# Kernel tuning notes

Hardware: AMD Instinct MI355X
Metric: run time of the kernel (lower is better)

## Reference

```python
import jax, jax.numpy as jnp
import numpy as np
import math

NUM_HEADS = 16
ATTN_WIDTH = 256


def setup_inputs() -> dict:
    key = jax.random.key(0)
    ks = jax.random.split(key, 5)
    B, S, C, H = 2, 2048, 1024, 1024
    scale = 0.02
    return {
        "x": jax.random.normal(ks[0], (B, S, C), dtype=jnp.float32),
        "Wq": jax.random.normal(ks[1], (C, H), dtype=jnp.float32) * scale,
        "Wk": jax.random.normal(ks[2], (C, H), dtype=jnp.float32) * scale,
        "Wv": jax.random.normal(ks[3], (C, H), dtype=jnp.float32) * scale,
        "Wo": jax.random.normal(ks[4], (H, C), dtype=jnp.float32) * scale,
    }


def reference(x, Wq, Wk, Wv, Wo):
    B, S, C = x.shape
    H = NUM_HEADS
    dh = Wq.shape[1] // H  # head dim; Q.size(-1) in torch code

    def split_heads(t):
        # [B, S, H*dh] -> [B, H, S, dh]
        return t.reshape(B, S, H, dh).transpose(0, 2, 1, 3)

    q = split_heads(x @ Wq)
    k = split_heads(x @ Wk)
    v = split_heads(x @ Wv)

    scores = jnp.einsum("bhqd,bhkd->bhqk", q, k) / math.sqrt(dh)
    # exp-shift (first 'softmax-like' step, unnormalized)
    scores = jnp.exp(scores - jnp.max(scores, axis=-1, keepdims=True))
    # banded mask: tril(attn_width//2 - 1).triu(-(attn_width//2))
    i = jnp.arange(S)[:, None]
    j = jnp.arange(S)[None, :]
    d = j - i
    half = ATTN_WIDTH // 2
    mask = (d <= half - 1) & (d >= -half)
    scores = jnp.where(mask, scores, 0.0)
    # second softmax over the masked exp-scores (zeros contribute exp(0)=1)
    weights = jax.nn.softmax(scores, axis=-1)

    out = jnp.einsum("bhqk,bhkd->bhqd", weights, v)  # [B, H, S, dh]
    out = out.transpose(0, 2, 1, 3).reshape(B, S, H * dh)
    return out @ Wo
```

## Files before the change

kernel.cpp:

```cpp
#include <hip/hip_runtime.h>
#include <math.h>

typedef __bf16 bf16_t;
typedef bf16_t bf16x8 __attribute__((ext_vector_type(8)));
typedef bf16_t bf16x4 __attribute__((ext_vector_type(4)));
typedef float f32x4 __attribute__((ext_vector_type(4)));

constexpr int S_ = 2048;
constexpr float SCALE = 0.125f;

#define MFMA_B16(a, b, c) __builtin_amdgcn_mfma_f32_16x16x32_bf16(a, b, c, 0, 0, 0)

#define WAIT_VM0() __builtin_amdgcn_s_waitcnt(0x0F70)
#define WAIT_VM2() __builtin_amdgcn_s_waitcnt(0x0F72)
#define WAIT_VM4() __builtin_amdgcn_s_waitcnt(0x0F74)
#define BARRIER()  __builtin_amdgcn_s_barrier()

typedef __attribute__((address_space(1))) const void* as1_cvp;
typedef __attribute__((address_space(3))) void* as3_vp;

__device__ __forceinline__ void gl2lds16(const void* g, void* l)
{
    __builtin_amdgcn_global_load_lds((as1_cvp)g, (as3_vp)l, 16, 0, 0);
}

#define SRC_SWZ8(lane) ((((lane) & 3) ^ (((lane) >> 3) & 3)) * 8)
#define RD_SWZ8(quad, l15) ((((quad) ^ (((l15) >> 1) & 3))) * 8)

__global__ __launch_bounds__(256) void prep(const float* __restrict__ x,
                                            const float* __restrict__ Wq,
                                            const float* __restrict__ Wk,
                                            const float* __restrict__ Wv,
                                            const float* __restrict__ Wo,
                                            bf16_t* __restrict__ xb,
                                            bf16_t* __restrict__ Wqt,
                                            bf16_t* __restrict__ Wkt,
                                            bf16_t* __restrict__ Wvt,
                                            bf16_t* __restrict__ Wot,
                                            float* __restrict__ vsp)
{
    __shared__ float T[64][65];
    const int blk = blockIdx.x;
    const int tid = threadIdx.x;
    if (blk < 1024) {
#pragma unroll
        for (int u = 0; u < 4; ++u) {
            const int g = blk * 1024 + u * 256 + tid;
            const float4 v = ((const float4*)x)[g];
            bf16x4 o;
            o[0] = (bf16_t)v.x; o[1] = (bf16_t)v.y;
            o[2] = (bf16_t)v.z; o[3] = (bf16_t)v.w;
            *(bf16x4*)&xb[(size_t)g * 4] = o;
        }
    } else if (blk < 2048) {
        const int rem = blk - 1024;
        const int wsel = rem >> 8, t = rem & 255;
        const float* src = (wsel == 0) ? Wq : (wsel == 1) ? Wk : (wsel == 2) ? Wv : Wo;
        bf16_t* dst = (wsel == 0) ? Wqt : (wsel == 1) ? Wkt : (wsel == 2) ? Wvt : Wot;
        const int k0 = (t >> 4) * 64, n0 = (t & 15) * 64;
        const int rr = tid >> 4, c4 = (tid & 15) * 4;
#pragma unroll
        for (int u = 0; u < 4; ++u) {
            const float4 v = *(const float4*)&src[(size_t)(k0 + u * 16 + rr) * 1024 + n0 + c4];
            T[u * 16 + rr][c4 + 0] = v.x; T[u * 16 + rr][c4 + 1] = v.y;
            T[u * 16 + rr][c4 + 2] = v.z; T[u * 16 + rr][c4 + 3] = v.w;
        }
        __syncthreads();
#pragma unroll
        for (int u = 0; u < 4; ++u) {
            bf16x4 o;
#pragma unroll
            for (int e = 0; e < 4; ++e) o[e] = (bf16_t)T[c4 + e][u * 16 + rr];
            *(bf16x4*)&dst[(size_t)(n0 + u * 16 + rr) * 1024 + k0 + c4] = o;
        }
    } else {
#pragma unroll
        for (int u = 0; u < 8; ++u) vsp[u * 256 + tid] = 0.f;
    }
}

template <int MODE>
__device__ __forceinline__ void mfma_gemm_body(bf16_t* __restrict__ As,
                                               bf16_t* __restrict__ Bs,
                                               const bf16_t* __restrict__ A,
                                               const bf16_t* __restrict__ Bt,
                                               void* __restrict__ dst,
                                               float* __restrict__ vsum_out,
                                               int m0, int n0)
{
    const int tid = threadIdx.x;
    const int lane = tid & 63, wid = tid >> 6;
    const int l15 = lane & 15, quad = lane >> 4;
    const int wm = (wid & 1) * 64, wn = (wid >> 1) * 64;

    const int srow = wid * 32 + (lane >> 2);
    const int scg8 = SRC_SWZ8(lane);
    const bf16_t* Ag0 = A  + (size_t)(m0 + srow) * 1024 + scg8;
    const bf16_t* Ag1 = A  + (size_t)(m0 + srow + 16) * 1024 + scg8;
    const bf16_t* Bg0 = Bt + (size_t)(n0 + srow) * 1024 + scg8;
    const bf16_t* Bg1 = Bt + (size_t)(n0 + srow + 16) * 1024 + scg8;

    const int rs = RD_SWZ8(quad, l15);

    f32x4 acc[4][4];
#pragma unroll
    for (int i = 0; i < 4; ++i)
#pragma unroll
        for (int j = 0; j < 4; ++j) acc[i][j] = (f32x4){0.f, 0.f, 0.f, 0.f};

#pragma unroll
    for (int p = 0; p < 2; ++p) {
        const int k0 = p * 32;
        gl2lds16(Ag0 + k0, As + p * 4096 + (wid * 2 + 0) * 512);
        gl2lds16(Ag1 + k0, As + p * 4096 + (wid * 2 + 1) * 512);
        gl2lds16(Bg0 + k0, Bs + p * 4096 + (wid * 2 + 0) * 512);
        gl2lds16(Bg1 + k0, Bs + p * 4096 + (wid * 2 + 1) * 512);
    }

#pragma unroll
    for (int it = 0; it < 32; ++it) {
        if (it < 30) WAIT_VM4(); else WAIT_VM0();
        BARRIER();
        if (it < 30) {
            const int k0 = (it + 2) * 32;
            const int sb = (it + 2) % 3;
            gl2lds16(Ag0 + k0, As + sb * 4096 + (wid * 2 + 0) * 512);
            gl2lds16(Ag1 + k0, As + sb * 4096 + (wid * 2 + 1) * 512);
            gl2lds16(Bg0 + k0, Bs + sb * 4096 + (wid * 2 + 0) * 512);
            gl2lds16(Bg1 + k0, Bs + sb * 4096 + (wid * 2 + 1) * 512);
        }
        const int cb = it % 3;
        bf16x8 af[4], bfr[4];
#pragma unroll
        for (int mt = 0; mt < 4; ++mt)
            af[mt] = *(const bf16x8*)&As[cb * 4096 + (wm + mt * 16 + l15) * 32 + rs];
#pragma unroll
        for (int nt = 0; nt < 4; ++nt)
            bfr[nt] = *(const bf16x8*)&Bs[cb * 4096 + (wn + nt * 16 + l15) * 32 + rs];
#pragma unroll
        for (int mt = 0; mt < 4; ++mt)
#pragma unroll
            for (int nt = 0; nt < 4; ++nt)
                acc[mt][nt] = MFMA_B16(bfr[nt], af[mt], acc[mt][nt]);
    }

#pragma unroll
    for (int mt = 0; mt < 4; ++mt) {
        const int m = m0 + wm + mt * 16 + l15;
#pragma unroll
        for (int nt = 0; nt < 4; ++nt) {
            const int nb = n0 + wn + nt * 16 + quad * 4;
            if (MODE == 0) {
                *(f32x4*)&((float*)dst)[(size_t)m * 1024 + nb] = acc[mt][nt];
            } else if (MODE == 1) {
                const int bb = m >> 11, s = m & 2047;
                const int hh = nb >> 6, d = nb & 63;
                bf16x4 o;
#pragma unroll
                for (int u = 0; u < 4; ++u) o[u] = (bf16_t)acc[mt][nt][u];
                *(bf16x4*)&((bf16_t*)dst)[((size_t)(bb * 16 + hh) * 2048 + s) * 64 + d] = o;
            } else {
                const int bb = n0 >> 11;
                const int hh = m >> 6, dd = m & 63;
                bf16x4 o;
#pragma unroll
                for (int u = 0; u < 4; ++u) o[u] = (bf16_t)acc[mt][nt][u];
                *(bf16x4*)&((bf16_t*)dst)[((size_t)(bb * 16 + hh) * 64 + dd) * 2048 + (nb & 2047)] = o;
            }
        }
    }

    if (MODE == 2 && vsum_out != nullptr) {
        const int bb = n0 >> 11;
#pragma unroll
        for (int mt = 0; mt < 4; ++mt) {
            float p = 0.f;
#pragma unroll
            for (int nt = 0; nt < 4; ++nt)
                p += acc[mt][nt][0] + acc[mt][nt][1] + acc[mt][nt][2] + acc[mt][nt][3];
            p += __shfl_xor(p, 16);
            p += __shfl_xor(p, 32);
            if (quad == 0) {
                const int m = m0 + wm + mt * 16 + l15;
                atomicAdd(&vsum_out[(bb * 16 + (m >> 6)) * 64 + (m & 63)], p);
            }
        }
    }
}

__device__ __forceinline__ int remap_m(void) { return (blockIdx.x << 2) + (blockIdx.y >> 3); }
__device__ __forceinline__ int remap_n(void) { return blockIdx.y & 7; }

__global__ __launch_bounds__(256) void gemm_qkv_mfma(const bf16_t* __restrict__ xb,
                                                     const bf16_t* __restrict__ Wqt,
                                                     const bf16_t* __restrict__ Wkt,
                                                     const bf16_t* __restrict__ Wvt,
                                                     bf16_t* Qh, bf16_t* Kh, bf16_t* VhT,
                                                     float* vsp)
{
    __shared__ bf16_t As[12288];
    __shared__ bf16_t Bs[12288];
    if (blockIdx.z == 2) {
        mfma_gemm_body<2>(As, Bs, Wvt, xb, VhT, vsp, remap_n() * 128, remap_m() * 128);
    } else {
        const bf16_t* Bt = (blockIdx.z == 0) ? Wqt : Wkt;
        bf16_t* dst = (blockIdx.z == 0) ? Qh : Kh;
        mfma_gemm_body<1>(As, Bs, xb, Bt, dst, nullptr, remap_m() * 128, remap_n() * 128);
    }
}

__global__ __launch_bounds__(256) void gemm_out_mfma(const bf16_t* __restrict__ attn,
                                                     const bf16_t* __restrict__ Wot,
                                                     float* __restrict__ out)
{
    __shared__ bf16_t As[12288];
    __shared__ bf16_t Bs[12288];
    mfma_gemm_body<0>(As, Bs, attn, Wot, out, nullptr, remap_m() * 128, remap_n() * 128);
}

__global__ __launch_bounds__(256) void attn_k(const bf16_t* __restrict__ Qh,
                                              const bf16_t* __restrict__ Kh,
                                              const bf16_t* __restrict__ VhT,
                                              const float* __restrict__ vsp,
                                              bf16_t* __restrict__ attn)
{
    __shared__ bf16_t Qs[8192];
    __shared__ float mr_sh[128];
    __shared__ __align__(16) char uni[35328];

    bf16_t* KsB = (bf16_t*)uni;
    float*  msh = (float*)(uni + 32768);
    bf16_t* Ks2 = (bf16_t*)uni;
    bf16_t* VtL = (bf16_t*)(uni + 8192);
    bf16_t* Ws  = (bf16_t*)(uni + 16384);
    float*  zsh = (float*)(uni + 34816);

    const int tid = threadIdx.x;
    const int lane = tid & 63, wid = tid >> 6;
    const int l15 = lane & 15, quad = lane >> 4;

    const int f = blockIdx.x;
    const int seq = f >> 3;
    const int bh = (f & 7) + 8 * (seq >> 4);
    const int i0 = (seq & 15) * 128;
    const int b = bh >> 4, h = bh & 15;
    const bf16_t* Qb  = Qh  + (size_t)bh * 131072;
    const bf16_t* Kb  = Kh  + (size_t)bh * 131072;
    const bf16_t* VbT = VhT + (size_t)bh * 131072;

    const int ssw = SRC_SWZ8(lane);
    const int rs  = RD_SWZ8(quad, l15);

#pragma unroll
    for (int c = 0; c < 4; ++c) {
        const int gg = wid * 4 + c;
        const int half = gg >> 3;
        const int row = (gg & 7) * 16 + (lane >> 2);
        gl2lds16(Qb + (size_t)(i0 + row) * 64 + half * 32 + ssw, Qs + gg * 512);
    }
#pragma unroll
    for (int p = 0; p < 3; ++p)
#pragma unroll
        for (int c = 0; c < 2; ++c) {
            const int gg = wid * 2 + c;
            const int half = gg >> 2;
            const int row = (gg & 3) * 16 + (lane >> 2);
            gl2lds16(Kb + (size_t)(p * 64 + row) * 64 + half * 32 + ssw,
                     KsB + p * 4096 + gg * 512);
        }
    __syncthreads();

    bf16x8 af[8][2];
#pragma unroll
    for (int mt = 0; mt < 8; ++mt)
#pragma unroll
        for (int ks = 0; ks < 2; ++ks)
            af[mt][ks] = *(const bf16x8*)&Qs[ks * 4096 + (mt * 16 + l15) * 32 + rs];

    float vm[8];
#pragma unroll
    for (int mt = 0; mt < 8; ++mt) vm[mt] = -3.0e38f;

    for (int jc = 0; jc < 32; ++jc) {
        if (jc < 30) WAIT_VM4();
        else if (jc == 30) WAIT_VM2();
        else WAIT_VM0();
        BARRIER();
        if (jc < 29) {
            const int sb = (jc + 3) & 3;
#pragma unroll
            for (int c = 0; c < 2; ++c) {
                const int gg = wid * 2 + c;
                const int half = gg >> 2;
                const int row = (gg & 3) * 16 + (lane >> 2);
                gl2lds16(Kb + (size_t)((jc + 3) * 64 + row) * 64 + half * 32 + ssw,
                         KsB + sb * 4096 + gg * 512);
            }
        }
        const int cb = jc & 3;
        const bf16x8 b0 = *(const bf16x8*)&KsB[cb * 4096 + (wid * 16 + l15) * 32 + rs];
        const bf16x8 b1 = *(const bf16x8*)&KsB[cb * 4096 + 2048 + (wid * 16 + l15) * 32 + rs];
#pragma unroll
        for (int mt = 0; mt < 8; ++mt) {
            f32x4 t = (f32x4){0.f, 0.f, 0.f, 0.f};
            t = MFMA_B16(b0, af[mt][0], t);
            t = MFMA_B16(b1, af[mt][1], t);
            const float u = fmaxf(fmaxf(t[0], t[1]), t[2]);
            vm[mt] = fmaxf(fmaxf(u, t[3]), vm[mt]);
        }
    }

#pragma unroll
    for (int mt = 0; mt < 8; ++mt) {
        float v = vm[mt];
        v = fmaxf(v, __shfl_xor(v, 16));
        v = fmaxf(v, __shfl_xor(v, 32));
        if (quad == 0) msh[(wid * 8 + mt) * 16 + l15] = v;
    }
    __syncthreads();

    if (tid < 128) {
        const int mt = tid >> 4, il = tid & 15;
        const float v = fmaxf(fmaxf(msh[(0 * 8 + mt) * 16 + il], msh[(1 * 8 + mt) * 16 + il]),
                              fmaxf(msh[(2 * 8 + mt) * 16 + il], msh[(3 * 8 + mt) * 16 + il]));
        mr_sh[tid] = v * SCALE;
    }
    __syncthreads();

    bf16x8 aq[2][2];
#pragma unroll
    for (int t = 0; t < 2; ++t)
#pragma unroll
        for (int ks = 0; ks < 2; ++ks)
            aq[t][ks] = *(const bf16x8*)&Qs[ks * 4096 + ((wid * 2 + t) * 16 + l15) * 32 + rs];

    float mreg[2][4];
#pragma unroll
    for (int t = 0; t < 2; ++t)
#pragma unroll
        for (int r = 0; r < 4; ++r)
            mreg[t][r] = mr_sh[(wid * 2 + t) * 16 + quad * 4 + r];

    f32x4 vsd4[4];
#pragma unroll
    for (int dt = 0; dt < 4; ++dt)
        vsd4[dt] = *(const f32x4*)&vsp[bh * 64 + dt * 16 + quad * 4];

    f32x4 accO[2][4];
#pragma unroll
    for (int t = 0; t < 2; ++t)
#pragma unroll
        for (int dt = 0; dt < 4; ++dt) accO[t][dt] = (f32x4){0.f, 0.f, 0.f, 0.f};
    float zp[2][4] = {{0.f, 0.f, 0.f, 0.f}, {0.f, 0.f, 0.f, 0.f}};

    for (int cb2 = 0; cb2 < 6; ++cb2) {
        const int jb = i0 - 128 + cb2 * 64;
        if (jb < 0 || jb >= S_) continue;

        __syncthreads();
#pragma unroll
        for (int c = 0; c < 2; ++c) {
            const int gg = wid * 2 + c;
            const int half = gg >> 2;
            const int row = (gg & 3) * 16 + (lane >> 2);
            gl2lds16(Kb + (size_t)(jb + row) * 64 + half * 32 + ssw, Ks2 + gg * 512);
        }
#pragma unroll
        for (int c = 0; c < 2; ++c) {
            const int gg = wid * 2 + c;
            const int d = gg * 8 + (lane >> 3);
            const int jl = (lane & 7) ^ ((lane >> 3) & 7);
            gl2lds16(VbT + (size_t)d * 2048 + jb + jl * 8, VtL + gg * 512);
        }
        __syncthreads();

#pragma unroll
        for (int t = 0; t < 2; ++t) {
            const int mt = wid * 2 + t;
#pragma unroll
            for (int jt4 = 0; jt4 < 4; ++jt4) {
                const bf16x8 k0 = *(const bf16x8*)&Ks2[(jt4 * 16 + l15) * 32 + rs];
                const bf16x8 k1 = *(const bf16x8*)&Ks2[2048 + (jt4 * 16 + l15) * 32 + rs];
                f32x4 sc = (f32x4){0.f, 0.f, 0.f, 0.f};
                sc = MFMA_B16(aq[t][0], k0, sc);
                sc = MFMA_B16(aq[t][1], k1, sc);
#pragma unroll
                for (int r = 0; r < 4; ++r) {
                    const int ig = i0 + mt * 16 + quad * 4 + r;
                    const int jg = jb + jt4 * 16 + l15;
                    const int dd = jg - ig;
                    const bool ok = (dd >= -128) && (dd <= 127);
                    const float e1 = __expf(sc[r] * SCALE - mreg[t][r]);
                    const float wv = ok ? (__expf(e1) - 1.0f) : 0.0f;
                    const bf16_t wb = (bf16_t)wv;
                    zp[t][r] += (float)wb;
                    Ws[(mt * 16 + quad * 4 + r) * 72 + jt4 * 16 + l15] = wb;
                }
            }
        }
        __syncthreads();

#pragma unroll
        for (int ks = 0; ks < 2; ++ks) {
            bf16x8 bv[4];
#pragma unroll
            for (int dt = 0; dt < 4; ++dt)
                bv[dt] = *(const bf16x8*)&VtL[(dt * 16 + l15) * 64 +
                                              (((ks * 4 + quad) ^ (l15 & 7)) * 8)];
#pragma unroll
            for (int t = 0; t < 2; ++t) {
                const int mt = wid * 2 + t;
                const bf16x8 aw = *(const bf16x8*)&Ws[(mt * 16 + l15) * 72 + ks * 32 + quad * 8];
#pragma unroll
                for (int dt = 0; dt < 4; ++dt)
                    accO[t][dt] = MFMA_B16(bv[dt], aw, accO[t][dt]);
            }
        }
    }

#pragma unroll
    for (int t = 0; t < 2; ++t)
#pragma unroll
        for (int r = 0; r < 4; ++r) {
            float z = zp[t][r];
            z += __shfl_xor(z, 1);
            z += __shfl_xor(z, 2);
            z += __shfl_xor(z, 4);
            z += __shfl_xor(z, 8);
            if (l15 == 0) zsh[wid * 32 + t * 16 + quad * 4 + r] = z + (float)S_;
        }
    __syncthreads();

#pragma unroll
    for (int t = 0; t < 2; ++t) {
        const float rz = 1.0f / zsh[wid * 32 + t * 16 + l15];
        const int irow = i0 + (wid * 2 + t) * 16 + l15;
#pragma unroll
        for (int dt = 0; dt < 4; ++dt) {
            bf16x4 o;
#pragma unroll
            for (int r = 0; r < 4; ++r)
                o[r] = (bf16_t)((accO[t][dt][r] + vsd4[dt][r]) * rz);
            *(bf16x4*)&attn[(size_t)(b * S_ + irow) * 1024 + h * 64 + dt * 16 + quad * 4] = o;
        }
    }
}

extern "C" void kernel_launch(void* const* d_in, const int* in_sizes, int n_in,
                              void* d_out, int out_size, void* d_ws, size_t ws_size,
                              hipStream_t stream)
{
    const float* x  = (const float*)d_in[0];
    const float* Wq = (const float*)d_in[1];
    const float* Wk = (const float*)d_in[2];
    const float* Wv = (const float*)d_in[3];
    const float* Wo = (const float*)d_in[4];
    float* out = (float*)d_out;

    char* ws = (char*)d_ws;
    bf16_t* xb   = (bf16_t*)(ws + 0);
    bf16_t* Wqt  = (bf16_t*)(ws + 8388608);
    bf16_t* Wkt  = (bf16_t*)(ws + 10485760);
    bf16_t* Wvt  = (bf16_t*)(ws + 12582912);
    bf16_t* Wot  = (bf16_t*)(ws + 14680064);
    bf16_t* Qh   = (bf16_t*)(ws + 16777216);
    bf16_t* Kh   = (bf16_t*)(ws + 25165824);
    bf16_t* VhT  = (bf16_t*)(ws + 33554432);
    bf16_t* attn = (bf16_t*)(ws + 41943040);
    float*  vsp  = (float*)(ws + 50331648);

    prep<<<2049, 256, 0, stream>>>(x, Wq, Wk, Wv, Wo, xb, Wqt, Wkt, Wvt, Wot, vsp);
    gemm_qkv_mfma<<<dim3(8, 32, 3), 256, 0, stream>>>(xb, Wqt, Wkt, Wvt, Qh, Kh, VhT, vsp);
    attn_k<<<512, 256, 0, stream>>>(Qh, Kh, VhT, vsp, attn);
    gemm_out_mfma<<<dim3(8, 32), 256, 0, stream>>>(attn, Wot, out);
}
```

Measured before the change: 179.1 us.

## Double attention kernel block to 512 threads, splitting row and key tiles across waves

The attention kernel now launches 8 waves per block instead of 4. In the max pass, each wave covers 4 query tiles against one key tile. In the banded pass, each wave owns a single 16-row query tile. Load work per wave is halved, wait counts are adjusted to match, and the barrier between writing the weight tile and the PV MFMA is removed because each wave reads only its own rows. The aim is more waves in flight per CU and fewer registers per wave to hide latency. The cost is lower MFMA density per wave and more barrier participants.

```diff
diff --git a/kernel.cpp b/kernel.cpp
--- a/kernel.cpp
+++ b/kernel.cpp
@@ -12,6 +12,7 @@
 #define MFMA_B16(a, b, c) __builtin_amdgcn_mfma_f32_16x16x32_bf16(a, b, c, 0, 0, 0)
 
 #define WAIT_VM0() __builtin_amdgcn_s_waitcnt(0x0F70)
+#define WAIT_VM1() __builtin_amdgcn_s_waitcnt(0x0F71)
 #define WAIT_VM2() __builtin_amdgcn_s_waitcnt(0x0F72)
 #define WAIT_VM4() __builtin_amdgcn_s_waitcnt(0x0F74)
 #define BARRIER()  __builtin_amdgcn_s_barrier()
@@ -218,11 +219,11 @@
     mfma_gemm_body<0>(As, Bs, attn, Wot, out, nullptr, remap_m() * 128, remap_n() * 128);
 }
 
-__global__ __launch_bounds__(256) void attn_k(const bf16_t* __restrict__ Qh,
-                                              const bf16_t* __restrict__ Kh,
-                                              const bf16_t* __restrict__ VhT,
-                                              const float* __restrict__ vsp,
-                                              bf16_t* __restrict__ attn)
+__global__ __launch_bounds__(512, 4) void attn_k(const bf16_t* __restrict__ Qh,
+                                                 const bf16_t* __restrict__ Kh,
+                                                 const bf16_t* __restrict__ VhT,
+                                                 const float* __restrict__ vsp,
+                                                 bf16_t* __restrict__ attn)
 {
     __shared__ bf16_t Qs[8192];
     __shared__ float mr_sh[128];
@@ -252,56 +253,53 @@
     const int rs  = RD_SWZ8(quad, l15);
 
 #pragma unroll
-    for (int c = 0; c < 4; ++c) {
-        const int gg = wid * 4 + c;
+    for (int c = 0; c < 2; ++c) {
+        const int gg = wid * 2 + c;
         const int half = gg >> 3;
         const int row = (gg & 7) * 16 + (lane >> 2);
         gl2lds16(Qb + (size_t)(i0 + row) * 64 + half * 32 + ssw, Qs + gg * 512);
     }
 #pragma unroll
-    for (int p = 0; p < 3; ++p)
-#pragma unroll
-        for (int c = 0; c < 2; ++c) {
-            const int gg = wid * 2 + c;
-            const int half = gg >> 2;
-            const int row = (gg & 3) * 16 + (lane >> 2);
-            gl2lds16(Kb + (size_t)(p * 64 + row) * 64 + half * 32 + ssw,
-                     KsB + p * 4096 + gg * 512);
-        }
+    for (int p = 0; p < 3; ++p) {
+        const int gg = wid;
+        const int half = gg >> 2;
+        const int row = (gg & 3) * 16 + (lane >> 2);
+        gl2lds16(Kb + (size_t)(p * 64 + row) * 64 + half * 32 + ssw,
+                 KsB + p * 4096 + gg * 512);
+    }
     __syncthreads();
 
-    bf16x8 af[8][2];
-#pragma unroll
-    for (int mt = 0; mt < 8; ++mt)
+    const int itb = (wid & 1) * 4;
+    const int jt  = wid >> 1;
+    bf16x8 af[4][2];
+#pragma unroll
+    for (int mt = 0; mt < 4; ++mt)
 #pragma unroll
         for (int ks = 0; ks < 2; ++ks)
-            af[mt][ks] = *(const bf16x8*)&Qs[ks * 4096 + (mt * 16 + l15) * 32 + rs];
-
-    float vm[8];
-#pragma unroll
-    for (int mt = 0; mt < 8; ++mt) vm[mt] = -3.0e38f;
+            af[mt][ks] = *(const bf16x8*)&Qs[ks * 4096 + ((itb + mt) * 16 + l15) * 32 + rs];
+
+    float vm[4];
+#pragma unroll
+    for (int mt = 0; mt < 4; ++mt) vm[mt] = -3.0e38f;
 
     for (int jc = 0; jc < 32; ++jc) {
-        if (jc < 30) WAIT_VM4();
-        else if (jc == 30) WAIT_VM2();
+        if (jc < 30) WAIT_VM2();
+        else if (jc == 30) WAIT_VM1();
         else WAIT_VM0();
         BARRIER();
         if (jc < 29) {
             const int sb = (jc + 3) & 3;
-#pragma unroll
-            for (int c = 0; c < 2; ++c) {
-                const int gg = wid * 2 + c;
-                const int half = gg >> 2;
-                const int row = (gg & 3) * 16 + (lane >> 2);
-                gl2lds16(Kb + (size_t)((jc + 3) * 64 + row) * 64 + half * 32 + ssw,
-                         KsB + sb * 4096 + gg * 512);
-            }
+            const int gg = wid;
+            const int half = gg >> 2;
+            const int row = (gg & 3) * 16 + (lane >> 2);
+            gl2lds16(Kb + (size_t)((jc + 3) * 64 + row) * 64 + half * 32 + ssw,
+                     KsB + sb * 4096 + gg * 512);
         }
         const int cb = jc & 3;
-        const bf16x8 b0 = *(const bf16x8*)&KsB[cb * 4096 + (wid * 16 + l15) * 32 + rs];
-        const bf16x8 b1 = *(const bf16x8*)&KsB[cb * 4096 + 2048 + (wid * 16 + l15) * 32 + rs];
-#pragma unroll
-        for (int mt = 0; mt < 8; ++mt) {
+        const bf16x8 b0 = *(const bf16x8*)&KsB[cb * 4096 + (jt * 16 + l15) * 32 + rs];
+        const bf16x8 b1 = *(const bf16x8*)&KsB[cb * 4096 + 2048 + (jt * 16 + l15) * 32 + rs];
+#pragma unroll
+        for (int mt = 0; mt < 4; ++mt) {
             f32x4 t = (f32x4){0.f, 0.f, 0.f, 0.f};
             t = MFMA_B16(b0, af[mt][0], t);
             t = MFMA_B16(b1, af[mt][1], t);
@@ -311,63 +309,58 @@
     }
 
 #pragma unroll
-    for (int mt = 0; mt < 8; ++mt) {
+    for (int mt = 0; mt < 4; ++mt) {
         float v = vm[mt];
         v = fmaxf(v, __shfl_xor(v, 16));
         v = fmaxf(v, __shfl_xor(v, 32));
-        if (quad == 0) msh[(wid * 8 + mt) * 16 + l15] = v;
+        if (quad == 0) msh[wid * 64 + mt * 16 + l15] = v;
     }
     __syncthreads();
 
     if (tid < 128) {
         const int mt = tid >> 4, il = tid & 15;
-        const float v = fmaxf(fmaxf(msh[(0 * 8 + mt) * 16 + il], msh[(1 * 8 + mt) * 16 + il]),
-                              fmaxf(msh[(2 * 8 + mt) * 16 + il], msh[(3 * 8 + mt) * 16 + il]));
+        const int p = mt >> 2, lt = mt & 3;
+        const float v = fmaxf(fmaxf(msh[(0 + p) * 64 + lt * 16 + il],
+                                    msh[(2 + p) * 64 + lt * 16 + il]),
+                              fmaxf(msh[(4 + p) * 64 + lt * 16 + il],
+                                    msh[(6 + p) * 64 + lt * 16 + il]));
         mr_sh[tid] = v * SCALE;
     }
     __syncthreads();
 
-    bf16x8 aq[2][2];
-#pragma unroll
-    for (int t = 0; t < 2; ++t)
-#pragma unroll
-        for (int ks = 0; ks < 2; ++ks)
-            aq[t][ks] = *(const bf16x8*)&Qs[ks * 4096 + ((wid * 2 + t) * 16 + l15) * 32 + rs];
-
-    float mreg[2][4];
-#pragma unroll
-    for (int t = 0; t < 2; ++t)
-#pragma unroll
-        for (int r = 0; r < 4; ++r)
-            mreg[t][r] = mr_sh[(wid * 2 + t) * 16 + quad * 4 + r];
+    bf16x8 aq[2];
+#pragma unroll
+    for (int ks = 0; ks < 2; ++ks)
+        aq[ks] = *(const bf16x8*)&Qs[ks * 4096 + (wid * 16 + l15) * 32 + rs];
+
+    float mreg[4];
+#pragma unroll
+    for (int r = 0; r < 4; ++r)
+        mreg[r] = mr_sh[wid * 16 + quad * 4 + r];
 
     f32x4 vsd4[4];
 #pragma unroll
     for (int dt = 0; dt < 4; ++dt)
         vsd4[dt] = *(const f32x4*)&vsp[bh * 64 + dt * 16 + quad * 4];
 
-    f32x4 accO[2][4];
-#pragma unroll
-    for (int t = 0; t < 2; ++t)
-#pragma unroll
-        for (int dt = 0; dt < 4; ++dt) accO[t][dt] = (f32x4){0.f, 0.f, 0.f, 0.f};
-    float zp[2][4] = {{0.f, 0.f, 0.f, 0.f}, {0.f, 0.f, 0.f, 0.f}};
+    f32x4 accO[4];
+#pragma unroll
+    for (int dt = 0; dt < 4; ++dt) accO[dt] = (f32x4){0.f, 0.f, 0.f, 0.f};
+    float zp[4] = {0.f, 0.f, 0.f, 0.f};
 
     for (int cb2 = 0; cb2 < 6; ++cb2) {
         const int jb = i0 - 128 + cb2 * 64;
         if (jb < 0 || jb >= S_) continue;
 
         __syncthreads();
-#pragma unroll
-        for (int c = 0; c < 2; ++c) {
-            const int gg = wid * 2 + c;
+        {
+            const int gg = wid;
             const int half = gg >> 2;
             const int row = (gg & 3) * 16 + (lane >> 2);
             gl2lds16(Kb + (size_t)(jb + row) * 64 + half * 32 + ssw, Ks2 + gg * 512);
         }
-#pragma unroll
-        for (int c = 0; c < 2; ++c) {
-            const int gg = wid * 2 + c;
+        {
+            const int gg = wid;
             const int d = gg * 8 + (lane >> 3);
             const int jl = (lane & 7) ^ ((lane >> 3) & 7);
             gl2lds16(VbT + (size_t)d * 2048 + jb + jl * 8, VtL + gg * 512);
@@ -375,30 +368,25 @@
         __syncthreads();
 
 #pragma unroll
-        for (int t = 0; t < 2; ++t) {
-            const int mt = wid * 2 + t;
-#pragma unroll
-            for (int jt4 = 0; jt4 < 4; ++jt4) {
-                const bf16x8 k0 = *(const bf16x8*)&Ks2[(jt4 * 16 + l15) * 32 + rs];
-                const bf16x8 k1 = *(const bf16x8*)&Ks2[2048 + (jt4 * 16 + l15) * 32 + rs];
-                f32x4 sc = (f32x4){0.f, 0.f, 0.f, 0.f};
-                sc = MFMA_B16(aq[t][0], k0, sc);
-                sc = MFMA_B16(aq[t][1], k1, sc);
-#pragma unroll
-                for (int r = 0; r < 4; ++r) {
-                    const int ig = i0 + mt * 16 + quad * 4 + r;
-                    const int jg = jb + jt4 * 16 + l15;
-                    const int dd = jg - ig;
-                    const bool ok = (dd >= -128) && (dd <= 127);
-                    const float e1 = __expf(sc[r] * SCALE - mreg[t][r]);
-                    const float wv = ok ? (__expf(e1) - 1.0f) : 0.0f;
-                    const bf16_t wb = (bf16_t)wv;
-                    zp[t][r] += (float)wb;
-                    Ws[(mt * 16 + quad * 4 + r) * 72 + jt4 * 16 + l15] = wb;
-                }
+        for (int jt4 = 0; jt4 < 4; ++jt4) {
+            const bf16x8 k0 = *(const bf16x8*)&Ks2[(jt4 * 16 + l15) * 32 + rs];
+            const bf16x8 k1 = *(const bf16x8*)&Ks2[2048 + (jt4 * 16 + l15) * 32 + rs];
+            f32x4 sc = (f32x4){0.f, 0.f, 0.f, 0.f};
+            sc = MFMA_B16(aq[0], k0, sc);
+            sc = MFMA_B16(aq[1], k1, sc);
+#pragma unroll
+            for (int r = 0; r < 4; ++r) {
+                const int ig = i0 + wid * 16 + quad * 4 + r;
+                const int jg = jb + jt4 * 16 + l15;
+                const int dd = jg - ig;
+                const bool ok = (dd >= -128) && (dd <= 127);
+                const float e1 = __expf(sc[r] * SCALE - mreg[r]);
+                const float wv = ok ? (__expf(e1) - 1.0f) : 0.0f;
+                const bf16_t wb = (bf16_t)wv;
+                zp[r] += (float)wb;
+                Ws[(wid * 16 + quad * 4 + r) * 72 + jt4 * 16 + l15] = wb;
             }
         }
-        __syncthreads();
 
 #pragma unroll
         for (int ks = 0; ks < 2; ++ks) {
@@ -407,40 +395,33 @@
             for (int dt = 0; dt < 4; ++dt)
                 bv[dt] = *(const bf16x8*)&VtL[(dt * 16 + l15) * 64 +
                                               (((ks * 4 + quad) ^ (l15 & 7)) * 8)];
-#pragma unroll
-            for (int t = 0; t < 2; ++t) {
-                const int mt = wid * 2 + t;
-                const bf16x8 aw = *(const bf16x8*)&Ws[(mt * 16 + l15) * 72 + ks * 32 + quad * 8];
-#pragma unroll
-                for (int dt = 0; dt < 4; ++dt)
-                    accO[t][dt] = MFMA_B16(bv[dt], aw, accO[t][dt]);
-            }
-        }
-    }
-
-#pragma unroll
-    for (int t = 0; t < 2; ++t)
-#pragma unroll
-        for (int r = 0; r < 4; ++r) {
-            float z = zp[t][r];
-            z += __shfl_xor(z, 1);
-            z += __shfl_xor(z, 2);
-            z += __shfl_xor(z, 4);
-            z += __shfl_xor(z, 8);
-            if (l15 == 0) zsh[wid * 32 + t * 16 + quad * 4 + r] = z + (float)S_;
-        }
+            const bf16x8 aw = *(const bf16x8*)&Ws[(wid * 16 + l15) * 72 + ks * 32 + quad * 8];
+#pragma unroll
+            for (int dt = 0; dt < 4; ++dt)
+                accO[dt] = MFMA_B16(bv[dt], aw, accO[dt]);
+        }
+    }
+
+#pragma unroll
+    for (int r = 0; r < 4; ++r) {
+        float z = zp[r];
+        z += __shfl_xor(z, 1);
+        z += __shfl_xor(z, 2);
+        z += __shfl_xor(z, 4);
+        z += __shfl_xor(z, 8);
+        if (l15 == 0) zsh[wid * 16 + quad * 4 + r] = z + (float)S_;
+    }
     __syncthreads();
 
-#pragma unroll
-    for (int t = 0; t < 2; ++t) {
-        const float rz = 1.0f / zsh[wid * 32 + t * 16 + l15];
-        const int irow = i0 + (wid * 2 + t) * 16 + l15;
+    {
+        const float rz = 1.0f / zsh[wid * 16 + l15];
+        const int irow = i0 + wid * 16 + l15;
 #pragma unroll
         for (int dt = 0; dt < 4; ++dt) {
             bf16x4 o;
 #pragma unroll
             for (int r = 0; r < 4; ++r)
-                o[r] = (bf16_t)((accO[t][dt][r] + vsd4[dt][r]) * rz);
+                o[r] = (bf16_t)((accO[dt][r] + vsd4[dt][r]) * rz);
             *(bf16x4*)&attn[(size_t)(b * S_ + irow) * 1024 + h * 64 + dt * 16 + quad * 4] = o;
         }
     }
@@ -471,6 +452,6 @@
 
     prep<<<2049, 256, 0, stream>>>(x, Wq, Wk, Wv, Wo, xb, Wqt, Wkt, Wvt, Wot, vsp);
     gemm_qkv_mfma<<<dim3(8, 32, 3), 256, 0, stream>>>(xb, Wqt, Wkt, Wvt, Qh, Kh, VhT, vsp);
-    attn_k<<<512, 256, 0, stream>>>(Qh, Kh, VhT, vsp, attn);
+    attn_k<<<512, 512, 0, stream>>>(Qh, Kh, VhT, vsp, attn);
     gemm_out_mfma<<<dim3(8, 32), 256, 0, stream>>>(attn, Wot, out);
 }
```

Measured after the change: 298.7 us. 66.8% more time.

## Load K fragments directly from global in row-max pass, drop LDS pipeline

Applied to the files above, without the earlier changes.

The full-row max pass now has each wave read its K MFMA fragments straight from global memory into registers with a one-step register prefetch. This replaces the 4-stage LDS ring buffer with async global-to-LDS copies and the per-iteration barriers. The MFMA section is wrapped in s_setprio to raise wave priority. The aim is to remove barrier synchronisation and the LDS round trip. In exchange, the global loads are less coalesced, latency is only hidden one iteration ahead, and each wave reads K separately.

```diff
diff --git a/kernel.cpp b/kernel.cpp
--- a/kernel.cpp
+++ b/kernel.cpp
@@ -228,8 +228,7 @@
     __shared__ float mr_sh[128];
     __shared__ __align__(16) char uni[35328];
 
-    bf16_t* KsB = (bf16_t*)uni;
-    float*  msh = (float*)(uni + 32768);
+    float*  msh = (float*)uni;
     bf16_t* Ks2 = (bf16_t*)uni;
     bf16_t* VtL = (bf16_t*)(uni + 8192);
     bf16_t* Ws  = (bf16_t*)(uni + 16384);
@@ -258,16 +257,6 @@
         const int row = (gg & 7) * 16 + (lane >> 2);
         gl2lds16(Qb + (size_t)(i0 + row) * 64 + half * 32 + ssw, Qs + gg * 512);
     }
-#pragma unroll
-    for (int p = 0; p < 3; ++p)
-#pragma unroll
-        for (int c = 0; c < 2; ++c) {
-            const int gg = wid * 2 + c;
-            const int half = gg >> 2;
-            const int row = (gg & 3) * 16 + (lane >> 2);
-            gl2lds16(Kb + (size_t)(p * 64 + row) * 64 + half * 32 + ssw,
-                     KsB + p * 4096 + gg * 512);
-        }
     __syncthreads();
 
     bf16x8 af[8][2];
@@ -281,33 +270,25 @@
 #pragma unroll
     for (int mt = 0; mt < 8; ++mt) vm[mt] = -3.0e38f;
 
+    const bf16_t* kf0 = Kb + (size_t)(wid * 16 + l15) * 64 + quad * 8;
+    bf16x8 k0 = *(const bf16x8*)(kf0);
+    bf16x8 k1 = *(const bf16x8*)(kf0 + 32);
+
     for (int jc = 0; jc < 32; ++jc) {
-        if (jc < 30) WAIT_VM4();
-        else if (jc == 30) WAIT_VM2();
-        else WAIT_VM0();
-        BARRIER();
-        if (jc < 29) {
-            const int sb = (jc + 3) & 3;
-#pragma unroll
-            for (int c = 0; c < 2; ++c) {
-                const int gg = wid * 2 + c;
-                const int half = gg >> 2;
-                const int row = (gg & 3) * 16 + (lane >> 2);
-                gl2lds16(Kb + (size_t)((jc + 3) * 64 + row) * 64 + half * 32 + ssw,
-                         KsB + sb * 4096 + gg * 512);
-            }
-        }
-        const int cb = jc & 3;
-        const bf16x8 b0 = *(const bf16x8*)&KsB[cb * 4096 + (wid * 16 + l15) * 32 + rs];
-        const bf16x8 b1 = *(const bf16x8*)&KsB[cb * 4096 + 2048 + (wid * 16 + l15) * 32 + rs];
+        const bf16_t* pn = kf0 + (size_t)((jc < 31) ? (jc + 1) : 31) * 4096;
+        const bf16x8 n0 = *(const bf16x8*)(pn);
+        const bf16x8 n1 = *(const bf16x8*)(pn + 32);
+        __builtin_amdgcn_s_setprio(1);
 #pragma unroll
         for (int mt = 0; mt < 8; ++mt) {
             f32x4 t = (f32x4){0.f, 0.f, 0.f, 0.f};
-            t = MFMA_B16(b0, af[mt][0], t);
-            t = MFMA_B16(b1, af[mt][1], t);
+            t = MFMA_B16(k0, af[mt][0], t);
+            t = MFMA_B16(k1, af[mt][1], t);
             const float u = fmaxf(fmaxf(t[0], t[1]), t[2]);
             vm[mt] = fmaxf(fmaxf(u, t[3]), vm[mt]);
         }
+        __builtin_amdgcn_s_setprio(0);
+        k0 = n0; k1 = n1;
     }
 
 #pragma unroll
@@ -379,11 +360,11 @@
             const int mt = wid * 2 + t;
 #pragma unroll
             for (int jt4 = 0; jt4 < 4; ++jt4) {
-                const bf16x8 k0 = *(const bf16x8*)&Ks2[(jt4 * 16 + l15) * 32 + rs];
-                const bf16x8 k1 = *(const bf16x8*)&Ks2[2048 + (jt4 * 16 + l15) * 32 + rs];
+                const bf16x8 kk0 = *(const bf16x8*)&Ks2[(jt4 * 16 + l15) * 32 + rs];
+                const bf16x8 kk1 = *(const bf16x8*)&Ks2[2048 + (jt4 * 16 + l15) * 32 + rs];
                 f32x4 sc = (f32x4){0.f, 0.f, 0.f, 0.f};
-                sc = MFMA_B16(aq[t][0], k0, sc);
-                sc = MFMA_B16(aq[t][1], k1, sc);
+                sc = MFMA_B16(aq[t][0], kk0, sc);
+                sc = MFMA_B16(aq[t][1], kk1, sc);
 #pragma unroll
                 for (int r = 0; r < 4; ++r) {
                     const int ig = i0 + mt * 16 + quad * 4 + r;
```

New measurement: 173.7 us (median of 2 runs). 3.0% less time.
